# Kernel tuning notes

Hardware: AMD Instinct MI355X
Metric: run time of the kernel (lower is better)

Reference implementation:

```python
import jax, jax.numpy as jnp
import numpy as np
from jax import lax

MAX_W = 4           # max_subword_block_width
DOWNSAMPLE = 2      # downsample_rate


def setup_inputs() -> dict:
    key = jax.random.key(0)
    k1, k2, k3, k4 = jax.random.split(key, 4)
    B, E, L, K = 8, 512, 4096, 5
    x = jax.random.normal(k1, (B, E, L), dtype=jnp.float32)
    conv_w = jax.random.normal(k2, (E, E, K), dtype=jnp.float32) * (1.0 / np.sqrt(E * K))
    conv_b = jax.random.normal(k3, (E,), dtype=jnp.float32) * 0.02
    score_w = jax.random.normal(k4, (E,), dtype=jnp.float32) * (1.0 / np.sqrt(E))
    return {"x": x, "conv_w": conv_w, "conv_b": conv_b, "score_w": score_w}


def reference(x, conv_w, conv_b, score_w):
    B, E, L = x.shape  # `length` captured BEFORE conv, as in the torch code
    # pre-GBST conv, VALID padding: length becomes L - K + 1
    y = lax.conv_general_dilated(
        x, conv_w, window_strides=(1,), padding='VALID',
        dimension_numbers=('NCH', 'OIH', 'NCH')) + conv_b[None, :, None]
    L2 = y.shape[-1]
    seqs, scores = [], []
    for w in range(1, MAX_W + 1):
        pad = (-L2) % w
        yp = jnp.pad(y, ((0, 0), (0, 0), (0, pad)))  # zero-pad to multiple of w
        nb = yp.shape[-1] // w
        pooled = yp.reshape(B, E, nb, w).mean(-1)          # avg_pool1d(kernel=w, stride=w)
        sc = jnp.einsum('ben,e->bn', pooled, score_w)      # Linear(E,1,bias=False)
        rs = jnp.repeat(pooled, w, axis=-1)                # repeat_interleave
        rsc = jnp.repeat(sc, w, axis=-1)
        cur = rs.shape[-1]
        if cur < L:  # re-pad with zeros up to the ORIGINAL (pre-conv) length
            rs = jnp.pad(rs, ((0, 0), (0, 0), (0, L - cur)))
            rsc = jnp.pad(rsc, ((0, 0), (0, L - cur)))
        seqs.append(rs[:, :, :L])
        scores.append(rsc[:, :L])
    S = jnp.stack(seqs, axis=-1)                           # [B,E,L,W]
    A = jax.nn.softmax(jnp.stack(scores, axis=-1), axis=-1)  # [B,L,W]
    out = jnp.einsum('belw,blw->bel', S, A)                # softmax-weighted combine
    r = DOWNSAMPLE
    Ld = (L // r) * r
    out = out[:, :, :Ld].reshape(B, E, L // r, r).mean(-1)  # final avg_pool1d
    return out
```

## Files before the change

### kernel.cpp

```cpp
#include <hip/hip_runtime.h>
#include <stdint.h>

#define E_DIM 512
#define L_IN  4096
#define L_OUT 4092
#define KW    5
#define B_DIM 8
#define L2P   4096
#define L_DS  2048
#define LP    4160

typedef __attribute__((ext_vector_type(8))) short short8;
typedef __attribute__((ext_vector_type(4))) float f32x4;

__device__ __forceinline__ unsigned short f2bf(float f) {
    uint32_t u = __float_as_uint(f);
    u += 0x7fffu + ((u >> 16) & 1);
    return (unsigned short)(u >> 16);
}
__device__ __forceinline__ float bf2f(unsigned short h) {
    return __uint_as_float((uint32_t)h << 16);
}

__global__ __launch_bounds__(256)
void xt_kernel(const float* __restrict__ x, unsigned short* __restrict__ Xt)
{
    const int b  = blockIdx.z;
    const int i0 = blockIdx.y * 64;
    const int l0 = blockIdx.x * 64;
    __shared__ float T[64][65];
    const int tid = threadIdx.x;

    const int ir = tid >> 4;
    const int cq = (tid & 15) * 4;
    #pragma unroll
    for (int jj = 0; jj < 4; ++jj) {
        int i = jj * 16 + ir;
        float4 v = make_float4(0.f, 0.f, 0.f, 0.f);
        if (l0 < L_IN)
            v = *reinterpret_cast<const float4*>(
                &x[((size_t)b * E_DIM + i0 + i) * L_IN + l0 + cq]);
        T[i][cq + 0] = v.x; T[i][cq + 1] = v.y;
        T[i][cq + 2] = v.z; T[i][cq + 3] = v.w;
    }
    __syncthreads();
    const int h  = tid & 31;
    const int rq = tid >> 5;
    #pragma unroll
    for (int j = 0; j < 8; ++j) {
        int lr = j * 8 + rq;
        ushort2 o;
        o.x = f2bf(T[2 * h][lr]);
        o.y = f2bf(T[2 * h + 1][lr]);
        *reinterpret_cast<ushort2*>(
            &Xt[((size_t)b * LP + l0 + lr) * E_DIM + i0 + 2 * h]) = o;
    }
}

__global__ __launch_bounds__(256)
void wt_kernel(const float* __restrict__ w, unsigned short* __restrict__ Wt)
{
    int idx = blockIdx.x * 256 + threadIdx.x;
    if (idx >= E_DIM * E_DIM) return;
    #pragma unroll
    for (int k = 0; k < KW; ++k)
        Wt[(size_t)k * E_DIM * E_DIM + idx] = f2bf(w[(size_t)idx * KW + k]);
}

#define XS_ROWS  272
#define XS_BYTES (XS_ROWS * 64)
#define N_XCH    (XS_BYTES / 1024)
#define WS_OFF   XS_BYTES
#define WS_BYTES (5 * 128 * 64)
#define LDS_BYTES (XS_BYTES + WS_BYTES)
#define N_CH     (LDS_BYTES / 1024)

__global__ __launch_bounds__(256, 2)
void conv_mfma(const unsigned short* __restrict__ Xt,
               const unsigned short* __restrict__ Wt,
               const float* __restrict__ bias,
               const float* __restrict__ sw,
               unsigned short* __restrict__ y,
               float* __restrict__ sp)
{
    __shared__ __align__(16) unsigned char lds[LDS_BYTES];
    const int l0 = blockIdx.x * 256;
    const int e0 = blockIdx.y * 128;
    const int b  = blockIdx.z;
    const int tid  = threadIdx.x;
    const int lane = tid & 63;
    const int wv   = tid >> 6;
    const int wr = wv >> 1, wc = wv & 1;
    const int lr = lane & 15, lg = lane >> 4;
    const int ln4r = lane >> 2;
    const int xswz = ((lane & 3) ^ ((lane >> 3) & 3)) * 8;

    const unsigned short* xt_base =
        Xt + ((size_t)b * LP + l0) * E_DIM + xswz;

    f32x4 acc[4][8] = {};

    for (int ks = 0; ks < 16; ++ks) {
        const int i0 = ks * 32;
        __syncthreads();
        for (int cch = wv; cch < N_CH; cch += 4) {
            void* lp = (void*)(lds + cch * 1024);
            const unsigned short* gp;
            if (cch < N_XCH) {
                int row = cch * 16 + ln4r;
                gp = xt_base + (size_t)row * E_DIM + i0;
            } else {
                int rk = (cch - N_XCH) * 16 + ln4r;
                int k = rk >> 7, er = rk & 127;
                gp = Wt + ((size_t)k * E_DIM + e0 + er) * E_DIM + i0 + xswz;
            }
            __builtin_amdgcn_global_load_lds(
                (const __attribute__((address_space(1))) void*)gp,
                (__attribute__((address_space(3))) void*)lp,
                16, 0, 0);
        }
        __syncthreads();

        #pragma unroll
        for (int j = 0; j < KW; ++j) {
            int kt = j + wv; if (kt >= KW) kt -= KW;
            const int aAddr = WS_OFF + (kt * 128 + wr * 64 + lr) * 64
                            + ((lg ^ ((lr >> 1) & 3)) << 4);
            const int rB = wc * 128 + lr + kt;
            const int bAddr = rB * 64 + ((lg ^ (((lr + kt) >> 1) & 3)) << 4);

            short8 aF[4], bF[8];
            #pragma unroll
            for (int m = 0; m < 4; ++m)
                aF[m] = *reinterpret_cast<const short8*>(&lds[aAddr + m * 1024]);
            #pragma unroll
            for (int n = 0; n < 8; ++n)
                bF[n] = *reinterpret_cast<const short8*>(&lds[bAddr + n * 1024]);
            #pragma unroll
            for (int m = 0; m < 4; ++m)
                #pragma unroll
                for (int n = 0; n < 8; ++n)
                    acc[m][n] = __builtin_amdgcn_mfma_f32_16x16x32_bf16(
                        aF[m], bF[n], acc[m][n], 0, 0, 0);
        }
    }

    float spn[8] = {};
    #pragma unroll
    for (int m = 0; m < 4; ++m)
        #pragma unroll
        for (int q = 0; q < 4; ++q) {
            int e = e0 + wr * 64 + m * 16 + lg * 4 + q;
            float bv = bias[e];
            float wv_s = sw[e];
            unsigned short* yr =
                y + ((size_t)b * E_DIM + e) * L2P + l0 + wc * 128 + lr;
            #pragma unroll
            for (int n = 0; n < 8; ++n) {
                float v = acc[m][n][q] + bv;
                yr[n * 16] = f2bf(v);
                spn[n] = fmaf(v, wv_s, spn[n]);
            }
        }
    #pragma unroll
    for (int n = 0; n < 8; ++n) {
        float p = spn[n];
        p += __shfl_xor(p, 16);
        p += __shfl_xor(p, 32);
        if (lane < 16) {
            int l = l0 + wc * 128 + n * 16 + lane;
            sp[((size_t)b * L2P + l) * 8 + blockIdx.y * 2 + wr] = p;
        }
    }
}

__global__ __launch_bounds__(256)
void weight_kernel(const float* __restrict__ sp, float* __restrict__ A)
{
    const int b  = blockIdx.y;
    const int l0 = blockIdx.x * 256;
    const int tid = threadIdx.x;
    __shared__ float sl[260];

    for (int idx = tid; idx < 260; idx += 256) {
        int l = l0 - 2 + idx;
        float v = 0.f;
        if (l >= 0 && l < L_OUT) {
            const float* p = &sp[((size_t)b * L2P + l) * 8];
            v = ((p[0] + p[1]) + (p[2] + p[3])) + ((p[4] + p[5]) + (p[6] + p[7]));
        }
        sl[idx] = v;
    }
    __syncthreads();

    const int l = l0 + tid;
    if (l >= L_OUT) return;
    #define SL(i) sl[(i) - (l0 - 2)]
    float sc0 = SL(l);
    int n2 = l & ~1;
    float sc1 = 0.5f * (SL(n2) + SL(n2 + 1));
    int n3 = (l / 3) * 3;
    float sc2 = (1.f / 3.f) * (SL(n3) + SL(n3 + 1) + SL(n3 + 2));
    int n4 = l & ~3;
    float sc3 = 0.25f * (SL(n4) + SL(n4 + 1) + SL(n4 + 2) + SL(n4 + 3));
    #undef SL

    float m  = fmaxf(fmaxf(sc0, sc1), fmaxf(sc2, sc3));
    float e0 = __expf(sc0 - m), e1 = __expf(sc1 - m);
    float e2 = __expf(sc2 - m), e3 = __expf(sc3 - m);
    float inv = 1.f / (e0 + e1 + e2 + e3);

    float4 av = make_float4(e0 * inv, e1 * inv, e2 * inv, e3 * inv);
    *reinterpret_cast<float4*>(&A[((size_t)b * L2P + l) * 4]) = av;
}

typedef __attribute__((ext_vector_type(8))) unsigned short u16x8;

__global__ __launch_bounds__(256)
void combine_kernel(const unsigned short* __restrict__ y,
                    const float* __restrict__ A, float* __restrict__ out)
{
    const int e = blockIdx.x;
    const int b = blockIdx.y;
    const int tid = threadIdx.x;
    __shared__ float ys[L2P];

    const unsigned short* yrow = y + ((size_t)b * E_DIM + e) * L2P;
    #pragma unroll
    for (int j = 0; j < 2; ++j) {
        int base = (tid + j * 256) * 8;
        u16x8 v = *reinterpret_cast<const u16x8*>(&yrow[base]);
        #pragma unroll
        for (int t = 0; t < 8; ++t) ys[base + t] = bf2f(v[t]);
    }
    __syncthreads();

    const float* Ab = A + (size_t)b * L2P * 4;
    float* orow = out + ((size_t)b * E_DIM + e) * L_DS;
    #pragma unroll
    for (int j = 0; j < 8; ++j) {
        int m = tid + j * 256;
        float acc = 0.f;
        #pragma unroll
        for (int r = 0; r < 2; ++r) {
            int l = 2 * m + r;
            if (l < L_OUT) {
                const float4 a4 = *reinterpret_cast<const float4*>(&Ab[l * 4]);
                float t = a4.x * ys[l];
                int n2 = l & ~1;
                t += a4.y * 0.5f * (ys[n2] + ys[n2 + 1]);
                int n3 = (l / 3) * 3;
                t += a4.z * (1.f / 3.f) * (ys[n3] + ys[n3 + 1] + ys[n3 + 2]);
                int n4 = l & ~3;
                t += a4.w * 0.25f * (ys[n4] + ys[n4 + 1] + ys[n4 + 2] + ys[n4 + 3]);
                acc += t;
            }
        }
        orow[m] = 0.5f * acc;
    }
}

extern "C" void kernel_launch(void* const* d_in, const int* in_sizes, int n_in,
                              void* d_out, int out_size, void* d_ws, size_t ws_size,
                              hipStream_t stream)
{
    const float* x  = (const float*)d_in[0];
    const float* w  = (const float*)d_in[1];
    const float* bb = (const float*)d_in[2];
    const float* sw = (const float*)d_in[3];
    float* out = (float*)d_out;

    unsigned short* Y = (unsigned short*)d_ws;
    float* SP = (float*)(Y + (size_t)B_DIM * E_DIM * L2P);
    float* A  = SP + (size_t)B_DIM * L2P * 8;
    unsigned short* Xt = (unsigned short*)(A + (size_t)B_DIM * L2P * 4);
    unsigned short* Wt = Xt + (size_t)B_DIM * LP * E_DIM;

    xt_kernel<<<dim3(LP / 64, E_DIM / 64, B_DIM), 256, 0, stream>>>(x, Xt);
    wt_kernel<<<dim3(E_DIM * E_DIM / 256), 256, 0, stream>>>(w, Wt);
    conv_mfma<<<dim3(L2P / 256, E_DIM / 128, B_DIM), 256, 0, stream>>>(Xt, Wt, bb, sw, Y, SP);
    weight_kernel<<<dim3(L2P / 256, B_DIM), 256, 0, stream>>>(SP, A);
    combine_kernel<<<dim3(E_DIM, B_DIM), 256, 0, stream>>>(Y, A, out);
}
```

Baseline: 116.8 us.

## Switch conv MFMA to 32x32x16 tiles with double-buffered LDS fragment reads

Replaces the 16x16x32 bf16 MFMA tiling with 32x32x16 instructions, so each wave computes a 64x128 tile as 2x4 accumulators of 16 floats. The K-loop is split into ten half-depth groups whose LDS fragment reads are software-pipelined across two register sets, so reads for the next group are issued while MFMAs run on the current one. The larger MFMA shape reads fewer LDS fragments per flop, and the pipelining is meant to hide LDS latency. The epilogue is rewritten for the 32x32 accumulator layout, and the swizzle indexing changes to match.

Result: slower. 123.3 us (+5.6%).

```diff
diff --git a/kernel.cpp b/kernel.cpp
--- a/kernel.cpp
+++ b/kernel.cpp
@@ -10,8 +10,8 @@
 #define L_DS  2048
 #define LP    4160
 
-typedef __attribute__((ext_vector_type(8))) short short8;
-typedef __attribute__((ext_vector_type(4))) float f32x4;
+typedef __attribute__((ext_vector_type(8)))  short short8;
+typedef __attribute__((ext_vector_type(16))) float f32x16;
 
 __device__ __forceinline__ unsigned short f2bf(float f) {
     uint32_t u = __float_as_uint(f);
@@ -75,6 +75,34 @@
 #define LDS_BYTES (XS_BYTES + WS_BYTES)
 #define N_CH     (LDS_BYTES / 1024)
 
+#define READG(g, aF, bF)                                                     \
+  {                                                                          \
+    const int kt_ = (g) >> 1, s_ = (g) & 1;                                  \
+    const int d_  = (s_ << 1) | hf;                                          \
+    _Pragma("unroll")                                                        \
+    for (int m_ = 0; m_ < 2; ++m_) {                                         \
+      const int r_ = kt_ * 128 + wr * 64 + m_ * 32 + lr32;                   \
+      aF[m_] = *reinterpret_cast<const short8*>(                             \
+          &lds[WS_OFF + r_ * 64 + ((d_ ^ ((lr32 >> 1) & 3)) << 4)]);         \
+    }                                                                        \
+    _Pragma("unroll")                                                        \
+    for (int n_ = 0; n_ < 4; ++n_) {                                         \
+      const int r_ = wc * 128 + n_ * 32 + lr32 + kt_;                        \
+      bF[n_] = *reinterpret_cast<const short8*>(                             \
+          &lds[r_ * 64 + ((d_ ^ ((r_ >> 1) & 3)) << 4)]);                    \
+    }                                                                        \
+  }
+
+#define MFMAG(aF, bF)                                                        \
+  {                                                                          \
+    _Pragma("unroll")                                                        \
+    for (int m_ = 0; m_ < 2; ++m_)                                           \
+      _Pragma("unroll")                                                      \
+      for (int n_ = 0; n_ < 4; ++n_)                                         \
+        acc[m_][n_] = __builtin_amdgcn_mfma_f32_32x32x16_bf16(               \
+            aF[m_], bF[n_], acc[m_][n_], 0, 0, 0);                           \
+  }
+
 __global__ __launch_bounds__(256, 2)
 void conv_mfma(const unsigned short* __restrict__ Xt,
                const unsigned short* __restrict__ Wt,
@@ -91,14 +119,14 @@
     const int lane = tid & 63;
     const int wv   = tid >> 6;
     const int wr = wv >> 1, wc = wv & 1;
-    const int lr = lane & 15, lg = lane >> 4;
+    const int lr32 = lane & 31, hf = lane >> 5;
     const int ln4r = lane >> 2;
     const int xswz = ((lane & 3) ^ ((lane >> 3) & 3)) * 8;
 
     const unsigned short* xt_base =
         Xt + ((size_t)b * LP + l0) * E_DIM + xswz;
 
-    f32x4 acc[4][8] = {};
+    f32x16 acc[2][4] = {};
 
     for (int ks = 0; ks < 16; ++ks) {
         const int i0 = ks * 32;
@@ -121,54 +149,39 @@
         }
         __syncthreads();
 
-        #pragma unroll
-        for (int j = 0; j < KW; ++j) {
-            int kt = j + wv; if (kt >= KW) kt -= KW;
-            const int aAddr = WS_OFF + (kt * 128 + wr * 64 + lr) * 64
-                            + ((lg ^ ((lr >> 1) & 3)) << 4);
-            const int rB = wc * 128 + lr + kt;
-            const int bAddr = rB * 64 + ((lg ^ (((lr + kt) >> 1) & 3)) << 4);
-
-            short8 aF[4], bF[8];
+        short8 aA[2], bA[4], aB[2], bB[4];
+        READG(0, aA, bA);
+        #pragma unroll
+        for (int gg = 0; gg < 5; ++gg) {
+            READG(2 * gg + 1, aB, bB);
+            MFMAG(aA, bA);
+            if (gg < 4) READG(2 * gg + 2, aA, bA);
+            MFMAG(aB, bB);
+        }
+    }
+
+    float spn[4] = {0.f, 0.f, 0.f, 0.f};
+    #pragma unroll
+    for (int m = 0; m < 2; ++m)
+        #pragma unroll
+        for (int r = 0; r < 16; ++r) {
+            const int e = e0 + wr * 64 + m * 32 + (r & 3) + 8 * (r >> 2) + 4 * hf;
+            const float bv = bias[e];
+            const float ws = sw[e];
+            unsigned short* yr =
+                y + ((size_t)b * E_DIM + e) * L2P + l0 + wc * 128 + lr32;
             #pragma unroll
-            for (int m = 0; m < 4; ++m)
-                aF[m] = *reinterpret_cast<const short8*>(&lds[aAddr + m * 1024]);
-            #pragma unroll
-            for (int n = 0; n < 8; ++n)
-                bF[n] = *reinterpret_cast<const short8*>(&lds[bAddr + n * 1024]);
-            #pragma unroll
-            for (int m = 0; m < 4; ++m)
-                #pragma unroll
-                for (int n = 0; n < 8; ++n)
-                    acc[m][n] = __builtin_amdgcn_mfma_f32_16x16x32_bf16(
-                        aF[m], bF[n], acc[m][n], 0, 0, 0);
-        }
-    }
-
-    float spn[8] = {};
-    #pragma unroll
-    for (int m = 0; m < 4; ++m)
-        #pragma unroll
-        for (int q = 0; q < 4; ++q) {
-            int e = e0 + wr * 64 + m * 16 + lg * 4 + q;
-            float bv = bias[e];
-            float wv_s = sw[e];
-            unsigned short* yr =
-                y + ((size_t)b * E_DIM + e) * L2P + l0 + wc * 128 + lr;
-            #pragma unroll
-            for (int n = 0; n < 8; ++n) {
-                float v = acc[m][n][q] + bv;
-                yr[n * 16] = f2bf(v);
-                spn[n] = fmaf(v, wv_s, spn[n]);
+            for (int n = 0; n < 4; ++n) {
+                float v = acc[m][n][r] + bv;
+                yr[n * 32] = f2bf(v);
+                spn[n] = fmaf(v, ws, spn[n]);
             }
         }
     #pragma unroll
-    for (int n = 0; n < 8; ++n) {
-        float p = spn[n];
-        p += __shfl_xor(p, 16);
-        p += __shfl_xor(p, 32);
-        if (lane < 16) {
-            int l = l0 + wc * 128 + n * 16 + lane;
+    for (int n = 0; n < 4; ++n) {
+        float p = spn[n] + __shfl_xor(spn[n], 32);
+        if (lane < 32) {
+            int l = l0 + wc * 128 + n * 32 + lane;
             sp[((size_t)b * L2P + l) * 8 + blockIdx.y * 2 + wr] = p;
         }
     }
```
